# Optimization experiments

Hardware: AMD Instinct MI355X
Metric: run time of the kernel (lower is better)

## Reference

```python
import jax, jax.numpy as jnp
import numpy as np

S = 64    # shapelets_size
N = 256   # num_shapelets
C = 3     # in_channels
B = 64
L = 2048


def setup_inputs() -> dict:
    key = jax.random.key(0)
    kx, ks = jax.random.split(key)
    x = jax.random.normal(kx, (B, C, L), dtype=jnp.float32)
    shapelets = jax.random.normal(ks, (C, N, S), dtype=jnp.float32)
    return {"x": x, "shapelets": shapelets}


def reference(x, shapelets):
    # x: (B, C, L); shapelets: (C, N, S)
    W = x.shape[2] - S + 1  # number of sliding windows
    # unfold: (B, C, W, S)
    idx = jnp.arange(W)[:, None] + jnp.arange(S)[None, :]
    win = x[:, :, idx]
    # cdist with mm-based euclidean: d^2 = |a|^2 + |b|^2 - 2 a.b
    win_sq = jnp.sum(win * win, axis=-1)                 # (B, C, W)
    shp_sq = jnp.sum(shapelets * shapelets, axis=-1)     # (C, N)
    cross = jnp.einsum('bcws,cns->bcwn', win, shapelets)  # (B, C, W, N)
    d2 = win_sq[..., None] + shp_sq[None, :, None, :] - 2.0 * cross
    d = jnp.sqrt(jnp.maximum(d2, 0.0))                   # (B, C, W, N)
    # sum over channels, keepdim -> (B, 1, W, N); transpose -> (B, 1, N, W); min over W
    summed = jnp.sum(d, axis=1, keepdims=True)
    out = jnp.min(jnp.swapaxes(summed, 2, 3), axis=3)    # (B, 1, N)
    return out
```

## Files before the change

### kernel.cpp

```cpp
#include <hip/hip_runtime.h>
#include <hip/hip_fp16.h>


typedef float  v4f __attribute__((ext_vector_type(4)));
typedef short  v8s __attribute__((ext_vector_type(8)));
typedef unsigned short u16;
typedef unsigned int   u32;
typedef unsigned long long u64;

#define S_ 64
#define N_ 256
#define C_ 3
#define B_ 64
#define L_ 2048
#define W_ 1985
#define NCHUNK 530
#define THREADS 1024
#define WAVES 16

__device__ __forceinline__ u16 f2bf(float f) {
    u32 u = __builtin_bit_cast(u32, f);
    return (u16)((u + 0x7FFFu + ((u >> 16) & 1u)) >> 16);
}
__device__ __forceinline__ float bf2f(u16 b) {
    return __builtin_bit_cast(float, ((u32)b) << 16);
}

__global__ __launch_bounds__(THREADS)
void shapelet_min_kernel(const float* __restrict__ x,
                         const float* __restrict__ shp,
                         float* __restrict__ out)
{
    __shared__ u64 xcopy[C_][4][NCHUNK];
    __shared__ __half wsq[C_][L_];

    const int tid  = threadIdx.x;
    const int wave = tid >> 6;
    const int lane = tid & 63;
    const int m    = lane & 15;
    const int q    = lane >> 4;
    const int ww   = wave >> 1;
    const int wn   = wave & 1;
    const int b    = blockIdx.x >> 2;
    const int n0   = (blockIdx.x & 3) << 6;

    u16* scratch = (u16*)&xcopy[0][0][0];
    #pragma unroll
    for (int k = 0; k < 3; ++k) {
        int idx = tid + k * THREADS;
        int sq = idx & 15;
        int n  = (idx >> 4) & 63;
        int c  = idx >> 10;
        v4f v = *(const v4f*)(shp + ((size_t)(c * N_ + n0 + n) * S_ + (sq << 2)));
        u64 pk = (u64)f2bf(v[0]) | ((u64)f2bf(v[1]) << 16)
               | ((u64)f2bf(v[2]) << 32) | ((u64)f2bf(v[3]) << 48);
        *(u64*)(scratch + ((c * 64 + n) * 72 + (sq << 2))) = pk;
    }
    __syncthreads();

    const float* xb = x + (size_t)b * (C_ * L_);
    float xf[2][8];
    int xc[2], xt[2];
    #pragma unroll
    for (int k = 0; k < 2; ++k) {
        int u = tid + k * THREADS;
        bool act = (u < C_ * NCHUNK);
        int uu = act ? u : 0;
        int c = uu / NCHUNK;
        int t = uu - c * NCHUNK;
        int e = t << 2;
        xc[k] = c; xt[k] = t;
        if (act && (e + 7 < L_)) {
            v4f a0 = *(const v4f*)(xb + c * L_ + e);
            v4f a1 = *(const v4f*)(xb + c * L_ + e + 4);
            xf[k][0] = a0[0]; xf[k][1] = a0[1]; xf[k][2] = a0[2]; xf[k][3] = a0[3];
            xf[k][4] = a1[0]; xf[k][5] = a1[1]; xf[k][6] = a1[2]; xf[k][7] = a1[3];
        } else {
            #pragma unroll
            for (int i = 0; i < 8; ++i)
                xf[k][i] = (act && (e + i < L_)) ? xb[c * L_ + e + i] : 0.f;
        }
    }

    v8s bfr[C_][2][2];
    float ssq[C_][2];
    #pragma unroll
    for (int c = 0; c < C_; ++c) {
        #pragma unroll
        for (int nt = 0; nt < 2; ++nt) {
            float sacc = 0.f;
            #pragma unroll
            for (int h = 0; h < 2; ++h) {
                v8s f = *(const v8s*)(scratch +
                         ((c * 64 + wn * 32 + nt * 16 + m) * 72 + h * 32 + q * 8));
                bfr[c][nt][h] = f;
                #pragma unroll
                for (int j = 0; j < 8; ++j) {
                    float e = bf2f((u16)f[j]);
                    sacc += e * e;
                }
            }
            sacc += __shfl_xor(sacc, 16);
            sacc += __shfl_xor(sacc, 32);
            ssq[c][nt] = sacc;
        }
    }
    __syncthreads();

    #pragma unroll
    for (int k = 0; k < 2; ++k) {
        int u = tid + k * THREADS;
        if (u < C_ * NCHUNK) {
            u16 w8[8];
            #pragma unroll
            for (int i = 0; i < 8; ++i) w8[i] = f2bf(-2.f * xf[k][i]);
            #pragma unroll
            for (int r = 0; r < 4; ++r) {
                u64 pk = (u64)w8[r] | ((u64)w8[r + 1] << 16)
                       | ((u64)w8[r + 2] << 32) | ((u64)w8[r + 3] << 48);
                xcopy[xc[k]][r][xt[k]] = pk;
            }
        }
    }
    __syncthreads();

    #pragma unroll
    for (int k = 0; k < 2; ++k) {
        int u = tid + k * THREADS;
        if (u < 512 * C_) {
            int c  = u >> 9;
            int t0 = u & 511;
            const u64* cp0 = &xcopy[c][0][0];
            u64 ch = cp0[t0];
            float h0 = bf2f((u16)ch),         h1 = bf2f((u16)(ch >> 16)),
                  h2 = bf2f((u16)(ch >> 32)), h3 = bf2f((u16)(ch >> 48));
            float s = h0 * h0 + h1 * h1 + h2 * h2 + h3 * h3;
            #pragma unroll
            for (int kk = 1; kk < 16; ++kk) {
                u64 c2 = cp0[t0 + kk];
                float e0 = bf2f((u16)c2),         e1 = bf2f((u16)(c2 >> 16)),
                      e2 = bf2f((u16)(c2 >> 32)), e3 = bf2f((u16)(c2 >> 48));
                s += e0 * e0; s += e1 * e1; s += e2 * e2; s += e3 * e3;
            }
            u64 ct = cp0[t0 + 16];
            float t4 = bf2f((u16)ct), t5 = bf2f((u16)(ct >> 16)), t6 = bf2f((u16)(ct >> 32));
            float s0 = s;
            float s1 = s0 - h0 * h0 + t4 * t4;
            float s2 = s1 - h1 * h1 + t5 * t5;
            float s3 = s2 - h2 * h2 + t6 * t6;
            union { u64 u; __half h[4]; } hp;
            hp.h[0] = __float2half(0.25f * s0); hp.h[1] = __float2half(0.25f * s1);
            hp.h[2] = __float2half(0.25f * s2); hp.h[3] = __float2half(0.25f * s3);
            *(u64*)&wsq[c][t0 << 2] = hp.u;
        }
    }
    __syncthreads();

    float mins[2] = {1e30f, 1e30f};
    const int r = m & 3;

    #pragma unroll 1
    for (int it = 0; it < 8; ++it) {
        const int wbase = it * 256 + ww * 32;
        if (wbase >= W_) continue;

        float sums[2][2][4];
        #pragma unroll
        for (int mt = 0; mt < 2; ++mt)
            #pragma unroll
            for (int nt = 0; nt < 2; ++nt)
                #pragma unroll
                for (int g = 0; g < 4; ++g) sums[mt][nt][g] = 0.f;

        #pragma unroll
        for (int c = 0; c < C_; ++c) {
            v8s afr[2][2];
            #pragma unroll
            for (int mt = 0; mt < 2; ++mt) {
                #pragma unroll
                for (int h = 0; h < 2; ++h) {
                    int p0 = wbase + mt * 16 + m + h * 32 + q * 8;
                    int T  = (p0 - r) >> 2;
                    const u64* cp = &xcopy[c][r][0];
                    union { u64 u[2]; v8s v; } tmp;
                    tmp.u[0] = cp[T];
                    tmp.u[1] = cp[T + 1];
                    afr[mt][h] = tmp.v;
                }
            }
            v4f acc[2][2];
            #pragma unroll
            for (int mt = 0; mt < 2; ++mt) {
                union { u64 u; __half h4[4]; } wq;
                wq.u = *(const u64*)&wsq[c][wbase + mt * 16 + q * 4];
                float wv[4];
                #pragma unroll
                for (int g = 0; g < 4; ++g) wv[g] = __half2float(wq.h4[g]);
                #pragma unroll
                for (int nt = 0; nt < 2; ++nt)
                    #pragma unroll
                    for (int g = 0; g < 4; ++g)
                        acc[mt][nt][g] = wv[g] + ssq[c][nt];
            }
            #pragma unroll
            for (int h = 0; h < 2; ++h)
                #pragma unroll
                for (int mt = 0; mt < 2; ++mt)
                    #pragma unroll
                    for (int nt = 0; nt < 2; ++nt)
                        acc[mt][nt] = __builtin_amdgcn_mfma_f32_16x16x32_bf16(
                            afr[mt][h], bfr[c][nt][h], acc[mt][nt], 0, 0, 0);

            #pragma unroll
            for (int mt = 0; mt < 2; ++mt)
                #pragma unroll
                for (int nt = 0; nt < 2; ++nt)
                    #pragma unroll
                    for (int g = 0; g < 4; ++g)
                        sums[mt][nt][g] += __builtin_amdgcn_sqrtf(fmaxf(acc[mt][nt][g], 0.f));
        }

        if (wbase + 31 < W_) {
            #pragma unroll
            for (int mt = 0; mt < 2; ++mt)
                #pragma unroll
                for (int nt = 0; nt < 2; ++nt)
                    #pragma unroll
                    for (int g = 0; g < 4; ++g)
                        mins[nt] = fminf(mins[nt], sums[mt][nt][g]);
        } else {
            #pragma unroll
            for (int mt = 0; mt < 2; ++mt)
                #pragma unroll
                for (int g = 0; g < 4; ++g) {
                    int w = wbase + mt * 16 + q * 4 + g;
                    bool ok = (w < W_);
                    #pragma unroll
                    for (int nt = 0; nt < 2; ++nt)
                        mins[nt] = fminf(mins[nt], ok ? sums[mt][nt][g] : 1e30f);
                }
        }
    }

    #pragma unroll
    for (int nt = 0; nt < 2; ++nt) {
        mins[nt] = fminf(mins[nt], __shfl_xor(mins[nt], 16));
        mins[nt] = fminf(mins[nt], __shfl_xor(mins[nt], 32));
    }
    __syncthreads();
    float* red = (float*)&wsq[0][0];
    if (lane < 16) {
        red[ww * 64 + wn * 32 + lane]      = mins[0];
        red[ww * 64 + wn * 32 + 16 + lane] = mins[1];
    }
    __syncthreads();
    if (tid < 64) {
        float v = red[tid];
        #pragma unroll
        for (int k = 1; k < 8; ++k) v = fminf(v, red[k * 64 + tid]);
        out[(size_t)b * N_ + n0 + tid] = v;
    }
}

extern "C" void kernel_launch(void* const* d_in, const int* in_sizes, int n_in,
                              void* d_out, int out_size, void* d_ws, size_t ws_size,
                              hipStream_t stream) {
    const float* x   = (const float*)d_in[0];
    const float* shp = (const float*)d_in[1];
    float* out       = (float*)d_out;
    hipLaunchKernelGGL(shapelet_min_kernel, dim3(256), dim3(THREADS), 0, stream,
                       x, shp, out);
}
```

Baseline: 85.60 us.

## Split window range across blocks and merge partial minima with atomicMin

The kernel now decomposes work by window quarter and shapelet half, launching 512 blocks instead of 256. Each block stages only its window slice in LDS and processes two 64-shapelet groups sequentially. It merges partial minima into global memory via an unsigned atomicMin after a memset that initializes the output to a large value. This is meant to raise parallelism and cut the per-block LDS footprint and redundant window-norm work, at the cost of an extra memset launch, atomics and halo recomputation per slice.

```diff
diff --git a/kernel.cpp b/kernel.cpp
--- a/kernel.cpp
+++ b/kernel.cpp
@@ -14,9 +14,10 @@
 #define B_ 64
 #define L_ 2048
 #define W_ 1985
-#define NCHUNK 530
+#define WQL 512
+#define NC 146
+#define CSTRIDE 160
 #define THREADS 1024
-#define WAVES 16
 
 __device__ __forceinline__ u16 f2bf(float f) {
     u32 u = __builtin_bit_cast(u32, f);
@@ -26,74 +27,117 @@
     return __builtin_bit_cast(float, ((u32)b) << 16);
 }
 
-__global__ __launch_bounds__(THREADS)
+__global__ __launch_bounds__(THREADS, 8)
 void shapelet_min_kernel(const float* __restrict__ x,
                          const float* __restrict__ shp,
                          float* __restrict__ out)
 {
-    __shared__ u64 xcopy[C_][4][NCHUNK];
-    __shared__ __half wsq[C_][L_];
+    __shared__ u64   xls[C_ * 4 * CSTRIDE];
+    __shared__ float wsq[C_][WQL];
+    __shared__ u16   scratch[C_ * 64 * 72];
+    __shared__ float red[16][64];
 
     const int tid  = threadIdx.x;
     const int wave = tid >> 6;
     const int lane = tid & 63;
     const int m    = lane & 15;
     const int q    = lane >> 4;
-    const int ww   = wave >> 1;
-    const int wn   = wave & 1;
-    const int b    = blockIdx.x >> 2;
-    const int n0   = (blockIdx.x & 3) << 6;
-
-    u16* scratch = (u16*)&xcopy[0][0][0];
+    const int ww   = wave & 3;
+    const int wn   = wave >> 2;
+    const int blk  = blockIdx.x;
+    const int wq   = blk & 3;
+    const int nh   = (blk >> 2) & 1;
+    const int b    = blk >> 3;
+    const int w0   = wq << 9;
+    const int wlen = min(WQL, W_ - w0);
+
+    const float* xb = x + (size_t)b * (C_ * L_);
+    float xf[8];
+    int xc = 0, xt = 0;
+    bool xact = (tid < C_ * NC);
+    if (xact) {
+        xc = tid / NC;
+        xt = tid - xc * NC;
+        int e = w0 + (xt << 2);
+        if (e + 7 < L_) {
+            v4f a0 = *(const v4f*)(xb + xc * L_ + e);
+            v4f a1 = *(const v4f*)(xb + xc * L_ + e + 4);
+            xf[0] = a0[0]; xf[1] = a0[1]; xf[2] = a0[2]; xf[3] = a0[3];
+            xf[4] = a1[0]; xf[5] = a1[1]; xf[6] = a1[2]; xf[7] = a1[3];
+        } else {
+            #pragma unroll
+            for (int i = 0; i < 8; ++i)
+                xf[i] = (e + i < L_) ? xb[xc * L_ + e + i] : 0.f;
+        }
+    }
+
+    const int nbase = nh << 7;
     #pragma unroll
     for (int k = 0; k < 3; ++k) {
         int idx = tid + k * THREADS;
         int sq = idx & 15;
         int n  = (idx >> 4) & 63;
         int c  = idx >> 10;
-        v4f v = *(const v4f*)(shp + ((size_t)(c * N_ + n0 + n) * S_ + (sq << 2)));
+        v4f v = *(const v4f*)(shp + ((size_t)(c * N_ + nbase + n) * S_ + (sq << 2)));
         u64 pk = (u64)f2bf(v[0]) | ((u64)f2bf(v[1]) << 16)
                | ((u64)f2bf(v[2]) << 32) | ((u64)f2bf(v[3]) << 48);
         *(u64*)(scratch + ((c * 64 + n) * 72 + (sq << 2))) = pk;
     }
+
+    if (xact) {
+        u16 w8[8];
+        #pragma unroll
+        for (int i = 0; i < 8; ++i) w8[i] = f2bf(-2.f * xf[i]);
+        #pragma unroll
+        for (int r = 0; r < 4; ++r) {
+            u64 pk = (u64)w8[r] | ((u64)w8[r + 1] << 16)
+                   | ((u64)w8[r + 2] << 32) | ((u64)w8[r + 3] << 48);
+            xls[(xc * 4 + r) * CSTRIDE + 4 * r + xt] = pk;
+        }
+    }
     __syncthreads();
 
-    const float* xb = x + (size_t)b * (C_ * L_);
-    float xf[2][8];
-    int xc[2], xt[2];
-    #pragma unroll
-    for (int k = 0; k < 2; ++k) {
-        int u = tid + k * THREADS;
-        bool act = (u < C_ * NCHUNK);
-        int uu = act ? u : 0;
-        int c = uu / NCHUNK;
-        int t = uu - c * NCHUNK;
-        int e = t << 2;
-        xc[k] = c; xt[k] = t;
-        if (act && (e + 7 < L_)) {
-            v4f a0 = *(const v4f*)(xb + c * L_ + e);
-            v4f a1 = *(const v4f*)(xb + c * L_ + e + 4);
-            xf[k][0] = a0[0]; xf[k][1] = a0[1]; xf[k][2] = a0[2]; xf[k][3] = a0[3];
-            xf[k][4] = a1[0]; xf[k][5] = a1[1]; xf[k][6] = a1[2]; xf[k][7] = a1[3];
-        } else {
-            #pragma unroll
-            for (int i = 0; i < 8; ++i)
-                xf[k][i] = (act && (e + i < L_)) ? xb[c * L_ + e + i] : 0.f;
-        }
-    }
-
-    v8s bfr[C_][2][2];
-    float ssq[C_][2];
-    #pragma unroll
-    for (int c = 0; c < C_; ++c) {
-        #pragma unroll
-        for (int nt = 0; nt < 2; ++nt) {
+    if (tid < 128 * C_) {
+        int c  = tid >> 7;
+        int t0 = tid & 127;
+        const u64* cp0 = &xls[(c * 4) * CSTRIDE];
+        u64 ch = cp0[t0];
+        float h0 = bf2f((u16)ch),         h1 = bf2f((u16)(ch >> 16)),
+              h2 = bf2f((u16)(ch >> 32)), h3 = bf2f((u16)(ch >> 48));
+        float sq0 = h0 * h0, sq1 = h1 * h1, sq2 = h2 * h2;
+        float s = sq0 + sq1 + sq2 + h3 * h3;
+        #pragma unroll
+        for (int kk = 1; kk < 16; ++kk) {
+            u64 c2 = cp0[t0 + kk];
+            float e0 = bf2f((u16)c2),         e1 = bf2f((u16)(c2 >> 16)),
+                  e2 = bf2f((u16)(c2 >> 32)), e3 = bf2f((u16)(c2 >> 48));
+            s += e0 * e0; s += e1 * e1; s += e2 * e2; s += e3 * e3;
+        }
+        u64 ct = cp0[t0 + 16];
+        float t4 = bf2f((u16)ct), t5 = bf2f((u16)(ct >> 16)), t6 = bf2f((u16)(ct >> 32));
+        float s0 = s;
+        float s1 = s0 - sq0 + t4 * t4;
+        float s2 = s1 - sq1 + t5 * t5;
+        float s3 = s2 - sq2 + t6 * t6;
+        v4f o = (v4f){0.25f * s0, 0.25f * s1, 0.25f * s2, 0.25f * s3};
+        *(v4f*)&wsq[c][t0 << 2] = o;
+    }
+
+    const int r  = m & 3;
+    const int sE = m >> 2;
+
+    #pragma unroll 1
+    for (int g = 0; g < 2; ++g) {
+        v8s bfr[C_][2];
+        float ssq[C_];
+        #pragma unroll
+        for (int c = 0; c < C_; ++c) {
             float sacc = 0.f;
             #pragma unroll
             for (int h = 0; h < 2; ++h) {
                 v8s f = *(const v8s*)(scratch +
-                         ((c * 64 + wn * 32 + nt * 16 + m) * 72 + h * 32 + q * 8));
-                bfr[c][nt][h] = f;
+                         ((c * 64 + wn * 16 + m) * 72 + h * 32 + q * 8));
+                bfr[c][h] = f;
                 #pragma unroll
                 for (int j = 0; j < 8; ++j) {
                     float e = bf2f((u16)f[j]);
@@ -102,163 +146,78 @@
             }
             sacc += __shfl_xor(sacc, 16);
             sacc += __shfl_xor(sacc, 32);
-            ssq[c][nt] = sacc;
-        }
-    }
-    __syncthreads();
-
-    #pragma unroll
-    for (int k = 0; k < 2; ++k) {
-        int u = tid + k * THREADS;
-        if (u < C_ * NCHUNK) {
-            u16 w8[8];
-            #pragma unroll
-            for (int i = 0; i < 8; ++i) w8[i] = f2bf(-2.f * xf[k][i]);
-            #pragma unroll
-            for (int r = 0; r < 4; ++r) {
-                u64 pk = (u64)w8[r] | ((u64)w8[r + 1] << 16)
-                       | ((u64)w8[r + 2] << 32) | ((u64)w8[r + 3] << 48);
-                xcopy[xc[k]][r][xt[k]] = pk;
-            }
-        }
-    }
-    __syncthreads();
-
-    #pragma unroll
-    for (int k = 0; k < 2; ++k) {
-        int u = tid + k * THREADS;
-        if (u < 512 * C_) {
-            int c  = u >> 9;
-            int t0 = u & 511;
-            const u64* cp0 = &xcopy[c][0][0];
-            u64 ch = cp0[t0];
-            float h0 = bf2f((u16)ch),         h1 = bf2f((u16)(ch >> 16)),
-                  h2 = bf2f((u16)(ch >> 32)), h3 = bf2f((u16)(ch >> 48));
-            float s = h0 * h0 + h1 * h1 + h2 * h2 + h3 * h3;
-            #pragma unroll
-            for (int kk = 1; kk < 16; ++kk) {
-                u64 c2 = cp0[t0 + kk];
-                float e0 = bf2f((u16)c2),         e1 = bf2f((u16)(c2 >> 16)),
-                      e2 = bf2f((u16)(c2 >> 32)), e3 = bf2f((u16)(c2 >> 48));
-                s += e0 * e0; s += e1 * e1; s += e2 * e2; s += e3 * e3;
-            }
-            u64 ct = cp0[t0 + 16];
-            float t4 = bf2f((u16)ct), t5 = bf2f((u16)(ct >> 16)), t6 = bf2f((u16)(ct >> 32));
-            float s0 = s;
-            float s1 = s0 - h0 * h0 + t4 * t4;
-            float s2 = s1 - h1 * h1 + t5 * t5;
-            float s3 = s2 - h2 * h2 + t6 * t6;
-            union { u64 u; __half h[4]; } hp;
-            hp.h[0] = __float2half(0.25f * s0); hp.h[1] = __float2half(0.25f * s1);
-            hp.h[2] = __float2half(0.25f * s2); hp.h[3] = __float2half(0.25f * s3);
-            *(u64*)&wsq[c][t0 << 2] = hp.u;
-        }
-    }
-    __syncthreads();
-
-    float mins[2] = {1e30f, 1e30f};
-    const int r = m & 3;
-
-    #pragma unroll 1
-    for (int it = 0; it < 8; ++it) {
-        const int wbase = it * 256 + ww * 32;
-        if (wbase >= W_) continue;
-
-        float sums[2][2][4];
-        #pragma unroll
-        for (int mt = 0; mt < 2; ++mt)
-            #pragma unroll
-            for (int nt = 0; nt < 2; ++nt)
-                #pragma unroll
-                for (int g = 0; g < 4; ++g) sums[mt][nt][g] = 0.f;
-
-        #pragma unroll
-        for (int c = 0; c < C_; ++c) {
-            v8s afr[2][2];
-            #pragma unroll
-            for (int mt = 0; mt < 2; ++mt) {
-                #pragma unroll
-                for (int h = 0; h < 2; ++h) {
-                    int p0 = wbase + mt * 16 + m + h * 32 + q * 8;
-                    int T  = (p0 - r) >> 2;
-                    const u64* cp = &xcopy[c][r][0];
-                    union { u64 u[2]; v8s v; } tmp;
-                    tmp.u[0] = cp[T];
-                    tmp.u[1] = cp[T + 1];
-                    afr[mt][h] = tmp.v;
+            ssq[c] = sacc;
+        }
+        __syncthreads();
+
+        float minv = 1e30f;
+        #pragma unroll 1
+        for (int it = 0; it < 8; ++it) {
+            const int wb = it * 64 + ww * 16;
+            if (wb >= wlen) continue;
+
+            float sums[4] = {0.f, 0.f, 0.f, 0.f};
+            #pragma unroll
+            for (int c = 0; c < C_; ++c) {
+                const u64* cp = &xls[(c * 4 + r) * CSTRIDE + 4 * r];
+                int T0 = (wb >> 2) + 2 * q + sE;
+                union { u64 u[2]; v8s v; } a0, a1;
+                a0.u[0] = cp[T0];     a0.u[1] = cp[T0 + 1];
+                a1.u[0] = cp[T0 + 8]; a1.u[1] = cp[T0 + 9];
+
+                v4f wv = *(const v4f*)&wsq[c][wb + (q << 2)];
+                v4f acc;
+                #pragma unroll
+                for (int gi = 0; gi < 4; ++gi) acc[gi] = wv[gi] + ssq[c];
+                acc = __builtin_amdgcn_mfma_f32_16x16x32_bf16(a0.v, bfr[c][0], acc, 0, 0, 0);
+                acc = __builtin_amdgcn_mfma_f32_16x16x32_bf16(a1.v, bfr[c][1], acc, 0, 0, 0);
+
+                #pragma unroll
+                for (int gi = 0; gi < 4; ++gi)
+                    sums[gi] += __builtin_amdgcn_sqrtf(fmaxf(acc[gi], 0.f));
+            }
+            if (wb + 16 <= wlen) {
+                #pragma unroll
+                for (int gi = 0; gi < 4; ++gi) minv = fminf(minv, sums[gi]);
+            } else {
+                #pragma unroll
+                for (int gi = 0; gi < 4; ++gi) {
+                    bool ok = (wb + (q << 2) + gi) < wlen;
+                    minv = fminf(minv, ok ? sums[gi] : 1e30f);
                 }
             }
-            v4f acc[2][2];
-            #pragma unroll
-            for (int mt = 0; mt < 2; ++mt) {
-                union { u64 u; __half h4[4]; } wq;
-                wq.u = *(const u64*)&wsq[c][wbase + mt * 16 + q * 4];
-                float wv[4];
-                #pragma unroll
-                for (int g = 0; g < 4; ++g) wv[g] = __half2float(wq.h4[g]);
-                #pragma unroll
-                for (int nt = 0; nt < 2; ++nt)
-                    #pragma unroll
-                    for (int g = 0; g < 4; ++g)
-                        acc[mt][nt][g] = wv[g] + ssq[c][nt];
-            }
-            #pragma unroll
-            for (int h = 0; h < 2; ++h)
-                #pragma unroll
-                for (int mt = 0; mt < 2; ++mt)
-                    #pragma unroll
-                    for (int nt = 0; nt < 2; ++nt)
-                        acc[mt][nt] = __builtin_amdgcn_mfma_f32_16x16x32_bf16(
-                            afr[mt][h], bfr[c][nt][h], acc[mt][nt], 0, 0, 0);
-
-            #pragma unroll
-            for (int mt = 0; mt < 2; ++mt)
-                #pragma unroll
-                for (int nt = 0; nt < 2; ++nt)
-                    #pragma unroll
-                    for (int g = 0; g < 4; ++g)
-                        sums[mt][nt][g] += __builtin_amdgcn_sqrtf(fmaxf(acc[mt][nt][g], 0.f));
-        }
-
-        if (wbase + 31 < W_) {
-            #pragma unroll
-            for (int mt = 0; mt < 2; ++mt)
-                #pragma unroll
-                for (int nt = 0; nt < 2; ++nt)
-                    #pragma unroll
-                    for (int g = 0; g < 4; ++g)
-                        mins[nt] = fminf(mins[nt], sums[mt][nt][g]);
-        } else {
-            #pragma unroll
-            for (int mt = 0; mt < 2; ++mt)
-                #pragma unroll
-                for (int g = 0; g < 4; ++g) {
-                    int w = wbase + mt * 16 + q * 4 + g;
-                    bool ok = (w < W_);
-                    #pragma unroll
-                    for (int nt = 0; nt < 2; ++nt)
-                        mins[nt] = fminf(mins[nt], ok ? sums[mt][nt][g] : 1e30f);
-                }
-        }
-    }
-
-    #pragma unroll
-    for (int nt = 0; nt < 2; ++nt) {
-        mins[nt] = fminf(mins[nt], __shfl_xor(mins[nt], 16));
-        mins[nt] = fminf(mins[nt], __shfl_xor(mins[nt], 32));
-    }
-    __syncthreads();
-    float* red = (float*)&wsq[0][0];
-    if (lane < 16) {
-        red[ww * 64 + wn * 32 + lane]      = mins[0];
-        red[ww * 64 + wn * 32 + 16 + lane] = mins[1];
-    }
-    __syncthreads();
-    if (tid < 64) {
-        float v = red[tid];
-        #pragma unroll
-        for (int k = 1; k < 8; ++k) v = fminf(v, red[k * 64 + tid]);
-        out[(size_t)b * N_ + n0 + tid] = v;
+        }
+
+        minv = fminf(minv, __shfl_xor(minv, 16));
+        minv = fminf(minv, __shfl_xor(minv, 32));
+
+        if (g == 0) {
+            #pragma unroll
+            for (int k = 0; k < 3; ++k) {
+                int idx = tid + k * THREADS;
+                int sq = idx & 15;
+                int n  = (idx >> 4) & 63;
+                int c  = idx >> 10;
+                v4f v = *(const v4f*)(shp +
+                        ((size_t)(c * N_ + nbase + 64 + n) * S_ + (sq << 2)));
+                u64 pk = (u64)f2bf(v[0]) | ((u64)f2bf(v[1]) << 16)
+                       | ((u64)f2bf(v[2]) << 32) | ((u64)f2bf(v[3]) << 48);
+                *(u64*)(scratch + ((c * 64 + n) * 72 + (sq << 2))) = pk;
+            }
+        }
+        if (lane < 16) red[wave][wn * 16 + lane] = minv;
+        __syncthreads();
+
+        if (tid < 64) {
+            int tn = tid >> 4;
+            float v = red[tn * 4 + 0][tid];
+            v = fminf(v, red[tn * 4 + 1][tid]);
+            v = fminf(v, red[tn * 4 + 2][tid]);
+            v = fminf(v, red[tn * 4 + 3][tid]);
+            atomicMin((u32*)out + ((size_t)b * N_ + nbase + (g << 6) + tid),
+                      __float_as_uint(v));
+        }
+        if (g == 0) __syncthreads();
     }
 }
 
@@ -268,6 +227,7 @@
     const float* x   = (const float*)d_in[0];
     const float* shp = (const float*)d_in[1];
     float* out       = (float*)d_out;
-    hipLaunchKernelGGL(shapelet_min_kernel, dim3(256), dim3(THREADS), 0, stream,
-                       x, shp, out);
-}
+    hipMemsetAsync(d_out, 0x7f, (size_t)B_ * N_ * sizeof(float), stream);
+    hipLaunchKernelGGL(shapelet_min_kernel, dim3(512), dim3(THREADS), 0, stream,
+                       x, shp, (float*)d_out);
+}
```

Measured after the change: 87.42 us. 1.02x slower.
